# Performance work log

Hardware: AMD Instinct MI355X
Metric: run time of the kernel (lower is better)

The kernel has to match this reference:

```python
import jax, jax.numpy as jnp
import numpy as np

B, T, D, L = 16, 2048, 512, 2


def setup_inputs() -> dict:
    key = jax.random.key(0)
    k1, k2, k3 = jax.random.split(key, 3)
    scale = 1.0 / np.sqrt(D)
    x = jax.random.normal(k1, (B, T, D), dtype=jnp.float32)
    Wx = jax.random.normal(k2, (L, D, 4 * D), dtype=jnp.float32) * scale
    Wh = jax.random.normal(k3, (L, D, 4 * D), dtype=jnp.float32) * scale
    b = jnp.zeros((L, 4 * D), dtype=jnp.float32)
    return {"x": x, "Wx": Wx, "Wh": Wh, "b": b}


def _lstm_layer(y, Wx_l, Wh_l, b_l):
    # y: [B, T, D]; Wx_l: [D, 4D]; Wh_l: [D, 4D]; b_l: [4D]
    Bn, Tn, Dn = y.shape
    # Precompute input contribution for all timesteps (one big GEMM).
    xg = jnp.einsum('btd,de->bte', y, Wx_l) + b_l  # [B, T, 4D]

    def step(carry, xt):
        h, c = carry
        gates = xt + h @ Wh_l  # [B, 4D]
        i, f, g, o = jnp.split(gates, 4, axis=-1)
        i = jax.nn.sigmoid(i)
        f = jax.nn.sigmoid(f)
        g = jnp.tanh(g)
        o = jax.nn.sigmoid(o)
        c = f * c + i * g
        h = o * jnp.tanh(c)
        return (h, c), h

    h0 = jnp.zeros((Bn, Dn), y.dtype)
    c0 = jnp.zeros((Bn, Dn), y.dtype)
    _, ys = jax.lax.scan(step, (h0, c0), jnp.swapaxes(xg, 0, 1))  # [T, B, D]
    return jnp.swapaxes(ys, 0, 1)


def reference(x, Wx, Wh, b):
    # Stacked LSTM with residual skip (flax LSTMCell gate order i, f, g, o;
    # input kernels have no bias, hidden kernels carry the bias -> single b).
    y = x
    for l in range(Wx.shape[0]):
        y = _lstm_layer(y, Wx[l], Wh[l], b[l])
    return y + x  # skip=1
```

## Files before the change

### kernel.cpp

```cpp
#include <hip/hip_runtime.h>
#include <stdint.h>

#define B_  16
#define T_  2048
#define D_  512

typedef short v8s __attribute__((ext_vector_type(8)));
typedef float v4f __attribute__((ext_vector_type(4)));

#define WT_OFF   0u
#define H0_OFF   8388608u
#define H1_OFF   41943040u
#define XB_OFF   75497472u
#define WS_NEED  (XB_OFF + 33554432u)

#define SENT 0xFFFFFFFFu

__device__ __forceinline__ short f2bf(float f) {
  unsigned u = __builtin_bit_cast(unsigned, f);
  u = (u + 0x7FFFu + ((u >> 16) & 1u)) >> 16;
  return (short)u;
}
__device__ __forceinline__ float sigmoid_fast(float z) { return 1.f / (1.f + __expf(-z)); }
__device__ __forceinline__ float tanh_fast(float z) {
  float e = __expf(2.f * z);
  return 1.f - 2.f / (e + 1.f);
}
__device__ __forceinline__ unsigned long long cohLoadU2(const unsigned* p) {
  return __hip_atomic_load((unsigned long long*)p, __ATOMIC_RELAXED, __HIP_MEMORY_SCOPE_AGENT);
}
__device__ __forceinline__ void cohStoreU(unsigned* p, unsigned v) {
  __hip_atomic_store(p, v, __ATOMIC_RELAXED, __HIP_MEMORY_SCOPE_AGENT);
}

__global__ void prep_weights(const float* __restrict__ Wx, const float* __restrict__ Wh,
                             short* __restrict__ wT) {
  int tid = blockIdx.x * 256 + threadIdx.x;
  int l   = tid >> 21;
  int mat = (tid >> 20) & 1;
  int rem = tid & ((1 << 20) - 1);
  int k   = rem >> 11;
  int col = rem & 2047;
  const float* src = mat ? Wh : Wx;
  float v = src[(l << 20) + (k << 11) + col];
  int q = col >> 9, r9 = col & 511, g = r9 >> 3, jj = r9 & 7;
  int c = q * 8 + jj, ntile = c >> 4, n = c & 15;
  int kap = k >> 5, k5 = k & 31, quad = k5 >> 3, j = k5 & 7;
  int lane = quad * 16 + n;
  int dst = ((((l * 2 + mat) * 64 + g) * 2 + ntile) * 16 + kap) * 512 + lane * 8 + j;
  wT[dst] = f2bf(v);
}

__global__ void prep_x(const float* __restrict__ x, short* __restrict__ xP,
                       unsigned* __restrict__ hwords) {
  int tid = blockIdx.x * 256 + threadIdx.x;
  hwords[tid] = SENT;
  int b = tid >> 20, r = tid & ((1 << 20) - 1), t = r >> 9, d = r & 511;
  xP[(size_t)t * 8192 + (d >> 3) * 128 + b * 8 + (d & 7)] = f2bf(x[tid]);
}

__device__ __forceinline__ unsigned coh_load8(const short* p, v8s afr[8]) {
  unsigned mx = 0;
#pragma unroll
  for (int kk = 0; kk < 8; ++kk) {
    const unsigned* q = (const unsigned*)(p + kk * 512);
    unsigned long long w0 = cohLoadU2(q);
    unsigned long long w1 = cohLoadU2(q + 2);
    unsigned a = (unsigned)w0, b = (unsigned)(w0 >> 32);
    unsigned c = (unsigned)w1, d = (unsigned)(w1 >> 32);
    mx = a > mx ? a : mx;
    mx = b > mx ? b : mx;
    mx = c > mx ? c : mx;
    mx = d > mx ? d : mx;
    uint4 pk; pk.x = a; pk.y = b; pk.z = c; pk.w = d;
    afr[kk] = __builtin_bit_cast(v8s, pk);
  }
  return mx;
}

__device__ __forceinline__ void mfma32(const v8s afr[8], const v8s wfr[4][8], v4f acc[4]) {
#pragma unroll
  for (int kk = 0; kk < 8; ++kk) {
#pragma unroll
    for (int nt = 0; nt < 4; ++nt)
      acc[nt] = __builtin_amdgcn_mfma_f32_16x16x32_bf16(afr[kk], wfr[nt][kk], acc[nt], 0, 0, 0);
  }
}

__global__ __launch_bounds__(256, 1) void lstm_persist(
    const float* __restrict__ x, const short* __restrict__ xP,
    const short* __restrict__ wT, const float* __restrict__ bias,
    short* h0, short* h1, float* __restrict__ out) {
  const int wg   = blockIdx.x;
  const int l    = wg >> 5;
  const int g    = wg & 31;
  const int tid  = threadIdx.x;
  const int wave = tid >> 6;
  const int lane = tid & 63;
  const int m    = wave >> 1;
  const int kh   = wave & 1;
  const int n15  = lane & 15;
  const int quad = lane >> 4;

  __shared__ float LDSG[2][4][16][76];

  short* hOwn = l ? h1 : h0;

  v8s wfr[4][8];
#pragma unroll
  for (int nt = 0; nt < 4; ++nt) {
    const int gOld = 2 * g + (nt >> 1);
    const int nt2  = nt & 1;
    const short* wb = wT + (size_t)((((l * 2 + m) * 64 + gOld) * 2 + nt2) * 16 + kh * 8) * 512 + lane * 8;
#pragma unroll
    for (int kk = 0; kk < 8; ++kk) wfr[nt][kk] = *(const v8s*)(wb + kk * 512);
  }

  const int eIdx = wave * 64 + lane;
  const int bb = eIdx >> 3, jp = eIdx & 7;
  const int hi = jp >> 2;
  const int jj = 2 * (jp & 3);
  float bq[4][2];
#pragma unroll
  for (int q = 0; q < 4; ++q) {
    bq[q][0] = bias[l * 2048 + q * 512 + g * 16 + 2 * jp];
    bq[q][1] = bias[l * 2048 + q * 512 + g * 16 + 2 * jp + 1];
  }
  float c0 = 0.f, c1 = 0.f;

  const int aOff = kh * 4096 + quad * 128 + n15 * 8;

  for (int t = 0; t < T_; ++t) {
    const int buf = t & 1;

    float2 xv;
    size_t xi = 0;
    if (l == 1 && wave < 2) {
      xi = (size_t)bb * (T_ * D_) + (size_t)t * D_ + g * 16 + 2 * jp;
      xv = *(const float2*)(x + xi);
    }

    v4f acc[4];
#pragma unroll
    for (int nt = 0; nt < 4; ++nt) acc[nt] = (v4f){0.f, 0.f, 0.f, 0.f};

    const short* hp = nullptr;
    if (m == 0) {
      if (l == 0) {
        const short* p = xP + (size_t)t * 8192 + aOff;
        v8s afr[8];
#pragma unroll
        for (int kk = 0; kk < 8; ++kk) afr[kk] = *(const v8s*)(p + kk * 512);
        mfma32(afr, wfr, acc);
      } else {
        hp = h0 + (size_t)t * 8192 + aOff;
      }
    } else if (t > 0) {
      hp = hOwn + (size_t)(t - 1) * 8192 + aOff;
    }

    if (hp) {
      v8s afr[8];
      if (m == 1) __builtin_amdgcn_s_sleep(12);
      unsigned mx = coh_load8(hp, afr);
      while (__ballot(mx == SENT) != 0) {
        __builtin_amdgcn_s_sleep(1);
        mx = coh_load8(hp, afr);
      }
      mfma32(afr, wfr, acc);
    }

#pragma unroll
    for (int nt = 0; nt < 4; ++nt) {
      const int rb = quad * 4;
#pragma unroll
      for (int r = 0; r < 4; ++r)
        LDSG[buf][wave][rb + r][nt * 16 + n15] = acc[nt][r];
    }
    __syncthreads();

    if (wave < 2) {
      float2 s[4];
#pragma unroll
      for (int q = 0; q < 4; ++q) {
        const int coff = (hi * 2 + (q >> 1)) * 16 + (q & 1) * 8 + jj;
        float2 a0 = *(const float2*)&LDSG[buf][0][bb][coff];
        float2 a1 = *(const float2*)&LDSG[buf][1][bb][coff];
        float2 a2 = *(const float2*)&LDSG[buf][2][bb][coff];
        float2 a3 = *(const float2*)&LDSG[buf][3][bb][coff];
        s[q].x = a0.x + a1.x + a2.x + a3.x + bq[q][0];
        s[q].y = a0.y + a1.y + a2.y + a3.y + bq[q][1];
      }
      float i0 = sigmoid_fast(s[0].x), i1 = sigmoid_fast(s[0].y);
      float f0 = sigmoid_fast(s[1].x), f1 = sigmoid_fast(s[1].y);
      float g0 = tanh_fast(s[2].x),    g1 = tanh_fast(s[2].y);
      float o0 = sigmoid_fast(s[3].x), o1 = sigmoid_fast(s[3].y);
      c0 = f0 * c0 + i0 * g0;
      c1 = f1 * c1 + i1 * g1;
      float h0v = o0 * tanh_fast(c0);
      float h1v = o1 * tanh_fast(c1);
      unsigned pack = (unsigned)(unsigned short)f2bf(h0v) |
                      ((unsigned)(unsigned short)f2bf(h1v) << 16);
      cohStoreU((unsigned*)hOwn + (size_t)t * 4096 + (2 * g + hi) * 64 + bb * 4 + (jp & 3), pack);
      if (l == 1) {
        float2 ov; ov.x = h0v + xv.x; ov.y = h1v + xv.y;
        *(float2*)(out + xi) = ov;
      }
    }
  }
}

extern "C" void kernel_launch(void* const* d_in, const int* in_sizes, int n_in,
                              void* d_out, int out_size, void* d_ws, size_t ws_size,
                              hipStream_t stream) {
  const float* x    = (const float*)d_in[0];
  const float* Wx   = (const float*)d_in[1];
  const float* Wh   = (const float*)d_in[2];
  const float* bias = (const float*)d_in[3];
  float* out = (float*)d_out;

  char* ws   = (char*)d_ws;
  short* wT  = (short*)(ws + WT_OFF);
  short* h0  = (short*)(ws + H0_OFF);
  short* h1  = (short*)(ws + H1_OFF);
  short* xP  = (short*)(ws + XB_OFF);
  unsigned* hwords = (unsigned*)(ws + H0_OFF);

  hipLaunchKernelGGL(prep_weights, dim3(16384), dim3(256), 0, stream, Wx, Wh, wT);
  hipLaunchKernelGGL(prep_x, dim3(65536), dim3(256), 0, stream, x, xP, hwords);
  hipLaunchKernelGGL(lstm_persist, dim3(64), dim3(256), 0, stream,
                     x, xP, wT, bias, h0, h1, out);
}
```

Measured before the change: 5.730 ms.

## Consume ready hidden-state chunks incrementally instead of waiting for full vector

Replaces the all-or-nothing polling of the previous hidden state with per-chunk readiness tracking. Each of the 8 K-chunks is fed to the MFMAs as soon as its whole wave sees no sentinel, and only chunks still pending are reloaded. The fixed s_sleep(12) before the first poll on the recurrent path is removed. This overlaps matrix work with waiting on slower producers, at the cost of more branching, per-chunk ballots, and possibly higher register pressure from the dynamic mask logic.

```diff
diff --git a/kernel.cpp b/kernel.cpp
--- a/kernel.cpp
+++ b/kernel.cpp
@@ -59,34 +59,6 @@
   xP[(size_t)t * 8192 + (d >> 3) * 128 + b * 8 + (d & 7)] = f2bf(x[tid]);
 }
 
-__device__ __forceinline__ unsigned coh_load8(const short* p, v8s afr[8]) {
-  unsigned mx = 0;
-#pragma unroll
-  for (int kk = 0; kk < 8; ++kk) {
-    const unsigned* q = (const unsigned*)(p + kk * 512);
-    unsigned long long w0 = cohLoadU2(q);
-    unsigned long long w1 = cohLoadU2(q + 2);
-    unsigned a = (unsigned)w0, b = (unsigned)(w0 >> 32);
-    unsigned c = (unsigned)w1, d = (unsigned)(w1 >> 32);
-    mx = a > mx ? a : mx;
-    mx = b > mx ? b : mx;
-    mx = c > mx ? c : mx;
-    mx = d > mx ? d : mx;
-    uint4 pk; pk.x = a; pk.y = b; pk.z = c; pk.w = d;
-    afr[kk] = __builtin_bit_cast(v8s, pk);
-  }
-  return mx;
-}
-
-__device__ __forceinline__ void mfma32(const v8s afr[8], const v8s wfr[4][8], v4f acc[4]) {
-#pragma unroll
-  for (int kk = 0; kk < 8; ++kk) {
-#pragma unroll
-    for (int nt = 0; nt < 4; ++nt)
-      acc[nt] = __builtin_amdgcn_mfma_f32_16x16x32_bf16(afr[kk], wfr[nt][kk], acc[nt], 0, 0, 0);
-  }
-}
-
 __global__ __launch_bounds__(256, 1) void lstm_persist(
     const float* __restrict__ x, const short* __restrict__ xP,
     const short* __restrict__ wT, const float* __restrict__ bias,
@@ -106,14 +78,14 @@
 
   short* hOwn = l ? h1 : h0;
 
-  v8s wfr[4][8];
+  v8s wfr[8][4];
 #pragma unroll
   for (int nt = 0; nt < 4; ++nt) {
     const int gOld = 2 * g + (nt >> 1);
     const int nt2  = nt & 1;
     const short* wb = wT + (size_t)((((l * 2 + m) * 64 + gOld) * 2 + nt2) * 16 + kh * 8) * 512 + lane * 8;
 #pragma unroll
-    for (int kk = 0; kk < 8; ++kk) wfr[nt][kk] = *(const v8s*)(wb + kk * 512);
+    for (int kk = 0; kk < 8; ++kk) wfr[kk][nt] = *(const v8s*)(wb + kk * 512);
   }
 
   const int eIdx = wave * 64 + lane;
@@ -151,7 +123,11 @@
         v8s afr[8];
 #pragma unroll
         for (int kk = 0; kk < 8; ++kk) afr[kk] = *(const v8s*)(p + kk * 512);
-        mfma32(afr, wfr, acc);
+#pragma unroll
+        for (int kk = 0; kk < 8; ++kk)
+#pragma unroll
+          for (int nt = 0; nt < 4; ++nt)
+            acc[nt] = __builtin_amdgcn_mfma_f32_16x16x32_bf16(afr[kk], wfr[kk][nt], acc[nt], 0, 0, 0);
       } else {
         hp = h0 + (size_t)t * 8192 + aOff;
       }
@@ -160,14 +136,49 @@
     }
 
     if (hp) {
-      v8s afr[8];
-      if (m == 1) __builtin_amdgcn_s_sleep(12);
-      unsigned mx = coh_load8(hp, afr);
-      while (__ballot(mx == SENT) != 0) {
+      v8s a[8];
+#pragma unroll
+      for (int kk = 0; kk < 8; ++kk) {
+        const unsigned* q = (const unsigned*)(hp + kk * 512);
+        unsigned long long w0 = cohLoadU2(q);
+        unsigned long long w1 = cohLoadU2(q + 2);
+        uint4 pk;
+        pk.x = (unsigned)w0; pk.y = (unsigned)(w0 >> 32);
+        pk.z = (unsigned)w1; pk.w = (unsigned)(w1 >> 32);
+        a[kk] = __builtin_bit_cast(v8s, pk);
+      }
+      unsigned need = 0xFFu;
+      for (;;) {
+#pragma unroll
+        for (int kk = 0; kk < 8; ++kk) {
+          if (need & (1u << kk)) {
+            uint4 u = __builtin_bit_cast(uint4, a[kk]);
+            unsigned mA = u.x > u.y ? u.x : u.y;
+            unsigned mB = u.z > u.w ? u.z : u.w;
+            unsigned mw = mA > mB ? mA : mB;
+            if (__ballot(mw == SENT) == 0ull) {
+#pragma unroll
+              for (int nt = 0; nt < 4; ++nt)
+                acc[nt] = __builtin_amdgcn_mfma_f32_16x16x32_bf16(a[kk], wfr[kk][nt], acc[nt], 0, 0, 0);
+              need &= ~(1u << kk);
+            }
+          }
+        }
+        if (!need) break;
+#pragma unroll
+        for (int kk = 0; kk < 8; ++kk) {
+          if (need & (1u << kk)) {
+            const unsigned* q = (const unsigned*)(hp + kk * 512);
+            unsigned long long w0 = cohLoadU2(q);
+            unsigned long long w1 = cohLoadU2(q + 2);
+            uint4 pk;
+            pk.x = (unsigned)w0; pk.y = (unsigned)(w0 >> 32);
+            pk.z = (unsigned)w1; pk.w = (unsigned)(w1 >> 32);
+            a[kk] = __builtin_bit_cast(v8s, pk);
+          }
+        }
         __builtin_amdgcn_s_sleep(1);
-        mx = coh_load8(hp, afr);
-      }
-      mfma32(afr, wfr, acc);
+      }
     }
 
 #pragma unroll
```

New measurement: 5.910 ms. +3.2%, slower.
